# Kernel optimization log

Measured on AMD Instinct MI355X. Metric: run time of the kernel, lower is better.

## Reference

```python
import jax, jax.numpy as jnp
import numpy as np

B, T, D = 2, 1024, 128
NEG_INF = -1e9


def setup_inputs() -> dict:
    key = jax.random.key(0)
    k_h, k_m, k_w = jax.random.split(key, 3)
    h = jax.random.normal(k_h, (B, T, D), dtype=jnp.float32)
    mask = jax.random.uniform(k_m, (B, T)) < 0.9  # bool [B, T]
    w = jax.random.normal(k_w, (D,), dtype=jnp.float32) * (1.0 / np.sqrt(D))  # Linear(dim,1,bias=False)
    return {"h": h, "mask": mask, "w": w}


def reference(h, mask, w):
    # wj[b, j] = W(h[b, j]) : score column scale, independent of i
    wj = jnp.einsum("btd,d->bt", h, w)  # [B, T]
    # pairwise L1 distance: dist[b, i, j] = sum_d |h[b,i,d] - h[b,j,d]|
    dist = jnp.abs(h[:, :, None, :] - h[:, None, :, :]).sum(-1)  # [B, T, T]
    score = -wj[:, None, :] * dist  # [B, T, T]
    score = jnp.where(mask[:, None, :], score, NEG_INF)
    alpha = jax.nn.softmax(score, axis=-1)  # [B, T, T]
    ctx = jnp.einsum("bij,bjd->bid", alpha, h)  # [B, T, D]
    return jnp.concatenate([h, ctx], axis=-1)  # [B, T, 2D]
```

## Files before the change

### kernel.cpp

```cpp
#include <hip/hip_runtime.h>
#include <math.h>

#define TT 1024
#define DD 128

static constexpr float kNegInf = -1e9f;

typedef __fp16 h2 __attribute__((ext_vector_type(2)));

__device__ __forceinline__ unsigned int pk16(float a, float b) {
  h2 v = __builtin_amdgcn_cvt_pkrtz(a, b);
  return __builtin_bit_cast(unsigned int, v);
}
__device__ __forceinline__ float dot2f(unsigned int a, unsigned int b, float c) {
#if __has_builtin(__builtin_amdgcn_fdot2)
  return __builtin_amdgcn_fdot2(__builtin_bit_cast(h2, a),
                                __builtin_bit_cast(h2, b), c, false);
#else
  h2 av = __builtin_bit_cast(h2, a), bv = __builtin_bit_cast(h2, b);
  return c + (float)av.x * (float)bv.x + (float)av.y * (float)bv.y;
#endif
}

__global__ __launch_bounds__(256) void k_prep(const float* __restrict__ h,
                                              const float* __restrict__ w,
                                              const int* __restrict__ mk,
                                              float* __restrict__ hTf,
                                              unsigned int* __restrict__ hT16,
                                              float* __restrict__ swj,
                                              float* __restrict__ bias) {
  __shared__ __align__(16) float tile[32][132];
  __shared__ float wred[32][8];
  const int b  = blockIdx.x >> 5;
  const int jt = blockIdx.x & 31;
  const int tid = threadIdx.x;
  const float4* src = (const float4*)h + (size_t)(b * TT + jt * 32) * 32;
#pragma unroll
  for (int k = 0; k < 4; ++k) {
    int idx = k * 256 + tid;
    float4 v = src[idx];
    int j = idx >> 5, c = idx & 31;
    *((float4*)&tile[j][c * 4]) = v;
  }
  __syncthreads();
#pragma unroll
  for (int k = 0; k < 4; ++k) {
    int idx = k * 256 + tid;
    int d = idx >> 3, jq = idx & 7;
    float4 v = {tile[jq * 4 + 0][d], tile[jq * 4 + 1][d],
                tile[jq * 4 + 2][d], tile[jq * 4 + 3][d]};
    *(float4*)&hTf[(size_t)(b * DD + d) * TT + jt * 32 + jq * 4] = v;
  }
#pragma unroll
  for (int k = 0; k < 2; ++k) {
    int idx = k * 256 + tid;
    int jp = idx >> 5, dq = idx & 31;
    uint4 wv;
    wv.x = pk16(tile[jp * 2][dq * 4 + 0], tile[jp * 2 + 1][dq * 4 + 0]);
    wv.y = pk16(tile[jp * 2][dq * 4 + 1], tile[jp * 2 + 1][dq * 4 + 1]);
    wv.z = pk16(tile[jp * 2][dq * 4 + 2], tile[jp * 2 + 1][dq * 4 + 2]);
    wv.w = pk16(tile[jp * 2][dq * 4 + 3], tile[jp * 2 + 1][dq * 4 + 3]);
    *(uint4*)&hT16[((size_t)(b * 512 + jt * 16 + jp)) * DD + dq * 4] = wv;
  }
  {
    const int j = tid & 31, dg = tid >> 5;
    float p = 0.f;
#pragma unroll
    for (int e = 0; e < 16; e += 4) {
      float4 hv = *(const float4*)&tile[j][dg * 16 + e];
      float4 wv = *(const float4*)&w[dg * 16 + e];
      p += hv.x * wv.x + hv.y * wv.y + hv.z * wv.z + hv.w * wv.w;
    }
    wred[j][dg] = p;
  }
  __syncthreads();
  if (tid < 32) {
    const int row = b * TT + jt * 32 + tid;
    float a = 0.f;
#pragma unroll
    for (int e = 0; e < 8; ++e) a += wred[tid][e];
    const bool ok = (mk[row] != 0);
    swj[row]  = ok ? -a : 0.f;
    bias[row] = ok ? 0.f : kNegInf;
  }
}

__global__ __launch_bounds__(256, 2) void k_fused(
    const float* __restrict__ h, const float* __restrict__ hTf,
    const unsigned int* __restrict__ hT16,
    const float* __restrict__ swj, const float* __restrict__ bias,
    float* __restrict__ out) {
  __shared__ __align__(16) float A_lds[4][DD];
  __shared__ __align__(16) unsigned int Pt[512][4];
  __shared__ __align__(16) float ctxp[4][4][DD];
  __shared__ float redm[4][4];
  __shared__ float redl[4][4];

  const int tid  = threadIdx.x;
  const int lane = tid & 63;
  const int wv   = tid >> 6;
  const int b    = blockIdx.x >> 8;
  const int row0 = (blockIdx.x & 255) * 4;
  const int rot  = blockIdx.x & 31;

  {
    const float2 v = *(const float2*)(h + ((size_t)b * TT + row0) * DD + tid * 2);
    *(float2*)&A_lds[0][tid * 2] = v;
  }
  __syncthreads();

  const int j = tid * 4;
  const float* Bb = hTf + (size_t)b * DD * TT + j;
  float acc[4][4];
#pragma unroll
  for (int u = 0; u < 4; ++u)
#pragma unroll
    for (int r = 0; r < 4; ++r) acc[u][r] = 0.f;

#define PS(s) (((s) + rot) & 31)

#define LOADB4(B, s) {                                        \
    B[0] = *(const float4*)(Bb + (size_t)((s) * 4 + 0) * TT); \
    B[1] = *(const float4*)(Bb + (size_t)((s) * 4 + 1) * TT); \
    B[2] = *(const float4*)(Bb + (size_t)((s) * 4 + 2) * TT); \
    B[3] = *(const float4*)(Bb + (size_t)((s) * 4 + 3) * TT); }

#define COMP4(B, s) {                                                  \
    _Pragma("unroll") for (int r = 0; r < 4; ++r) {                    \
      const float4 Ar = *(const float4*)&A_lds[r][(s) * 4];            \
      _Pragma("unroll") for (int e = 0; e < 4; ++e) {                  \
        const float a = (e == 0) ? Ar.x : (e == 1) ? Ar.y              \
                        : (e == 2) ? Ar.z : Ar.w;                      \
        acc[0][r] += fabsf(a - B[e].x);                                \
        acc[1][r] += fabsf(a - B[e].y);                                \
        acc[2][r] += fabsf(a - B[e].z);                                \
        acc[3][r] += fabsf(a - B[e].w);                                \
      } } }

  {
    float4 B0[4], B1[4];
    LOADB4(B0, PS(0));
#pragma unroll 1
    for (int s = 0; s < 16; ++s) {
      const int p1 = PS(2 * s + 1);
      const int p0 = PS(2 * s);
      LOADB4(B1, p1);
      COMP4(B0, p0);
      if (s < 15) LOADB4(B0, PS(2 * s + 2));
      COMP4(B1, p1);
    }
  }

  const float4 swv = *(const float4*)(swj + (size_t)b * TT + j);
  const float4 bvv = *(const float4*)(bias + (size_t)b * TT + j);
  float sc[4][4];
#pragma unroll
  for (int r = 0; r < 4; ++r) {
    sc[0][r] = fmaf(swv.x, acc[0][r], bvv.x);
    sc[1][r] = fmaf(swv.y, acc[1][r], bvv.y);
    sc[2][r] = fmaf(swv.z, acc[2][r], bvv.z);
    sc[3][r] = fmaf(swv.w, acc[3][r], bvv.w);
  }

  {
    float mr[4];
#pragma unroll
    for (int r = 0; r < 4; ++r) {
      float m0 = fmaxf(fmaxf(sc[0][r], sc[1][r]), fmaxf(sc[2][r], sc[3][r]));
#pragma unroll
      for (int off = 32; off; off >>= 1) m0 = fmaxf(m0, __shfl_xor(m0, off));
      mr[r] = m0;
    }
    if (lane == 0) {
#pragma unroll
      for (int r = 0; r < 4; ++r) redm[wv][r] = mr[r];
    }
  }
  __syncthreads();
  float M[4];
#pragma unroll
  for (int r = 0; r < 4; ++r)
    M[r] = fmaxf(fmaxf(redm[0][r], redm[1][r]),
                 fmaxf(redm[2][r], redm[3][r]));

  {
    float p[4][4];
    float ls[4] = {0.f, 0.f, 0.f, 0.f};
#pragma unroll
    for (int u = 0; u < 4; ++u)
#pragma unroll
      for (int r = 0; r < 4; ++r) {
        p[u][r] = __expf(sc[u][r] - M[r]);
        ls[r] += p[u][r];
      }
    uint4 w0 = {pk16(p[0][0], p[1][0]), pk16(p[0][1], p[1][1]),
                pk16(p[0][2], p[1][2]), pk16(p[0][3], p[1][3])};
    uint4 w1 = {pk16(p[2][0], p[3][0]), pk16(p[2][1], p[3][1]),
                pk16(p[2][2], p[3][2]), pk16(p[2][3], p[3][3])};
    *(uint4*)&Pt[tid * 2 + 0][0] = w0;
    *(uint4*)&Pt[tid * 2 + 1][0] = w1;
#pragma unroll
    for (int r = 0; r < 4; ++r) {
#pragma unroll
      for (int off = 32; off; off >>= 1) ls[r] += __shfl_xor(ls[r], off);
    }
    if (lane == 0) {
#pragma unroll
      for (int r = 0; r < 4; ++r) redl[wv][r] = ls[r];
    }
  }
  __syncthreads();

  const int dp = tid & 63;
  const int s  = tid >> 6;
  const unsigned int* Vp =
      hT16 + ((size_t)(b * 512 + s * 128)) * DD + dp * 2;
  float cx[4][2];
#pragma unroll
  for (int r = 0; r < 4; ++r) { cx[r][0] = 0.f; cx[r][1] = 0.f; }
  const int qrot = rot * 4;
#pragma unroll 4
  for (int qq = 0; qq < 128; ++qq) {
    const int q = (qq + qrot) & 127;
    const uint4 P = *(const uint4*)&Pt[s * 128 + q][0];
    const uint2 V = *(const uint2*)(Vp + (size_t)q * DD);
    cx[0][0] = dot2f(P.x, V.x, cx[0][0]); cx[0][1] = dot2f(P.x, V.y, cx[0][1]);
    cx[1][0] = dot2f(P.y, V.x, cx[1][0]); cx[1][1] = dot2f(P.y, V.y, cx[1][1]);
    cx[2][0] = dot2f(P.z, V.x, cx[2][0]); cx[2][1] = dot2f(P.z, V.y, cx[2][1]);
    cx[3][0] = dot2f(P.w, V.x, cx[3][0]); cx[3][1] = dot2f(P.w, V.y, cx[3][1]);
  }
#pragma unroll
  for (int r = 0; r < 4; ++r)
    *(float2*)&ctxp[s][r][dp * 2] = make_float2(cx[r][0], cx[r][1]);
  __syncthreads();

#pragma unroll
  for (int k = 0; k < 2; ++k) {
    const int idx = tid + k * 256;
    const int r = idx >> 7, d = idx & 127;
    const float L = redl[0][r] + redl[1][r] + redl[2][r] + redl[3][r];
    const float c = (ctxp[0][r][d] + ctxp[1][r][d]) +
                    (ctxp[2][r][d] + ctxp[3][r][d]);
    const size_t row = (size_t)blockIdx.x * 4 + r;
    out[row * 256 + d]       = A_lds[r][d];
    out[row * 256 + 128 + d] = c / L;
  }
}

extern "C" void kernel_launch(void* const* d_in, const int* in_sizes, int n_in,
                              void* d_out, int out_size, void* d_ws, size_t ws_size,
                              hipStream_t stream) {
  const float* h  = (const float*)d_in[0];
  const int*   mk = (const int*)d_in[1];
  const float* w  = (const float*)d_in[2];
  float* out = (float*)d_out;

  char* ws = (char*)d_ws;
  float*        swj  = (float*)ws;
  float*        bias = (float*)(ws + 8192);
  float*        hTf  = (float*)(ws + 16384);
  unsigned int* hT16 = (unsigned int*)(ws + 16384 + 1048576);

  hipLaunchKernelGGL(k_prep,  dim3(64),  dim3(256), 0, stream,
                     h, w, mk, hTf, hT16, swj, bias);
  hipLaunchKernelGGL(k_fused, dim3(512), dim3(256), 0, stream,
                     h, hTf, hT16, swj, bias, out);
}
```

Measured before the change: 41.13 us.

## Split fused kernel to exploit L1-distance symmetry via materialized score matrix

The fused distance-plus-softmax kernel is split into a score kernel and a softmax/context kernel. The score kernel computes only the upper-triangular blocks of the symmetric pairwise L1 distance. It writes both the score and its transpose (scaled by the row weight) into a global TxT score buffer. The softmax kernel then reads scores from that buffer. This roughly halves the distance arithmetic but adds an extra launch and about 8 MB of global writes and reads, plus scattered transposed stores.

```diff
diff --git a/kernel.cpp b/kernel.cpp
--- a/kernel.cpp
+++ b/kernel.cpp
@@ -85,57 +85,59 @@
   }
 }
 
-__global__ __launch_bounds__(256, 2) void k_fused(
+__global__ __launch_bounds__(256) void k_score(
     const float* __restrict__ h, const float* __restrict__ hTf,
-    const unsigned int* __restrict__ hT16,
     const float* __restrict__ swj, const float* __restrict__ bias,
-    float* __restrict__ out) {
+    float* __restrict__ S) {
   __shared__ __align__(16) float A_lds[4][DD];
-  __shared__ __align__(16) unsigned int Pt[512][4];
-  __shared__ __align__(16) float ctxp[4][4][DD];
-  __shared__ float redm[4][4];
-  __shared__ float redl[4][4];
-
-  const int tid  = threadIdx.x;
-  const int lane = tid & 63;
-  const int wv   = tid >> 6;
-  const int b    = blockIdx.x >> 8;
-  const int row0 = (blockIdx.x & 255) * 4;
-  const int rot  = blockIdx.x & 31;
-
-  {
-    const float2 v = *(const float2*)(h + ((size_t)b * TT + row0) * DD + tid * 2);
+
+  const int tid = threadIdx.x;
+  int t = blockIdx.x;
+  const int b = (t >= 384) ? 1 : 0;
+  t -= b * 384;
+  const int jh = (t < 128) ? 0 : 1;
+  const int rp = (t < 128) ? t : (t - 128);
+  const int i0 = rp * 4;
+  const int off = (jh == 0) ? i0 : ((i0 > 512) ? (i0 - 512) : 0);
+  const int jstart = jh * 512 + off;
+  const int nq = (512 - off) >> 2;
+  const int rot = blockIdx.x & 31;
+
+  {
+    const float2 v = *(const float2*)(h + ((size_t)b * TT + i0) * DD + tid * 2);
     *(float2*)&A_lds[0][tid * 2] = v;
   }
   __syncthreads();
 
-  const int j = tid * 4;
+  const int q  = tid & 127;
+  const int g2 = (tid >> 7) * 2;
+  if (q >= nq) return;
+  const int j = jstart + q * 4;
   const float* Bb = hTf + (size_t)b * DD * TT + j;
-  float acc[4][4];
-#pragma unroll
-  for (int u = 0; u < 4; ++u)
-#pragma unroll
-    for (int r = 0; r < 4; ++r) acc[u][r] = 0.f;
+
+  float acc[4][2];
+#pragma unroll
+  for (int u = 0; u < 4; ++u) { acc[u][0] = 0.f; acc[u][1] = 0.f; }
 
 #define PS(s) (((s) + rot) & 31)
-
 #define LOADB4(B, s) {                                        \
     B[0] = *(const float4*)(Bb + (size_t)((s) * 4 + 0) * TT); \
     B[1] = *(const float4*)(Bb + (size_t)((s) * 4 + 1) * TT); \
     B[2] = *(const float4*)(Bb + (size_t)((s) * 4 + 2) * TT); \
     B[3] = *(const float4*)(Bb + (size_t)((s) * 4 + 3) * TT); }
-
-#define COMP4(B, s) {                                                  \
-    _Pragma("unroll") for (int r = 0; r < 4; ++r) {                    \
-      const float4 Ar = *(const float4*)&A_lds[r][(s) * 4];            \
-      _Pragma("unroll") for (int e = 0; e < 4; ++e) {                  \
-        const float a = (e == 0) ? Ar.x : (e == 1) ? Ar.y              \
-                        : (e == 2) ? Ar.z : Ar.w;                      \
-        acc[0][r] += fabsf(a - B[e].x);                                \
-        acc[1][r] += fabsf(a - B[e].y);                                \
-        acc[2][r] += fabsf(a - B[e].z);                                \
-        acc[3][r] += fabsf(a - B[e].w);                                \
-      } } }
+#define COMP2(B, s) {                                                  \
+    const float4 A0 = *(const float4*)&A_lds[g2][(s) * 4];             \
+    const float4 A1 = *(const float4*)&A_lds[g2 + 1][(s) * 4];         \
+    _Pragma("unroll") for (int e = 0; e < 4; ++e) {                    \
+      const float a0 = (e == 0) ? A0.x : (e == 1) ? A0.y               \
+                       : (e == 2) ? A0.z : A0.w;                       \
+      const float a1 = (e == 0) ? A1.x : (e == 1) ? A1.y               \
+                       : (e == 2) ? A1.z : A1.w;                       \
+      acc[0][0] += fabsf(a0 - B[e].x); acc[0][1] += fabsf(a1 - B[e].x);\
+      acc[1][0] += fabsf(a0 - B[e].y); acc[1][1] += fabsf(a1 - B[e].y);\
+      acc[2][0] += fabsf(a0 - B[e].z); acc[2][1] += fabsf(a1 - B[e].z);\
+      acc[3][0] += fabsf(a0 - B[e].w); acc[3][1] += fabsf(a1 - B[e].w);\
+    } }
 
   {
     float4 B0[4], B1[4];
@@ -145,21 +147,66 @@
       const int p1 = PS(2 * s + 1);
       const int p0 = PS(2 * s);
       LOADB4(B1, p1);
-      COMP4(B0, p0);
+      COMP2(B0, p0);
       if (s < 15) LOADB4(B0, PS(2 * s + 2));
-      COMP4(B1, p1);
+      COMP2(B1, p1);
     }
   }
 
   const float4 swv = *(const float4*)(swj + (size_t)b * TT + j);
   const float4 bvv = *(const float4*)(bias + (size_t)b * TT + j);
+  float* Sb = S + (size_t)b * TT * TT;
+#pragma unroll
+  for (int r = 0; r < 2; ++r) {
+    float4 dv;
+    dv.x = fmaf(swv.x, acc[0][r], bvv.x);
+    dv.y = fmaf(swv.y, acc[1][r], bvv.y);
+    dv.z = fmaf(swv.z, acc[2][r], bvv.z);
+    dv.w = fmaf(swv.w, acc[3][r], bvv.w);
+    *(float4*)&Sb[(size_t)(i0 + g2 + r) * TT + j] = dv;
+  }
+  const float swi0 = swj[b * TT + i0 + g2];
+  const float swi1 = swj[b * TT + i0 + g2 + 1];
+  const float bii0 = bias[b * TT + i0 + g2];
+  const float bii1 = bias[b * TT + i0 + g2 + 1];
+#pragma unroll
+  for (int u = 0; u < 4; ++u) {
+    float2 tv;
+    tv.x = fmaf(swi0, acc[u][0], bii0);
+    tv.y = fmaf(swi1, acc[u][1], bii1);
+    *(float2*)&Sb[(size_t)(j + u) * TT + i0 + g2] = tv;
+  }
+}
+
+__global__ __launch_bounds__(256, 2) void k_sm(
+    const float* __restrict__ h, const float* __restrict__ S,
+    const unsigned int* __restrict__ hT16, float* __restrict__ out) {
+  __shared__ __align__(16) float A_lds[4][DD];
+  __shared__ __align__(16) unsigned int Pt[512][4];
+  __shared__ __align__(16) float ctxp[4][4][DD];
+  __shared__ float redm[4][4];
+  __shared__ float redl[4][4];
+
+  const int tid  = threadIdx.x;
+  const int lane = tid & 63;
+  const int wv   = tid >> 6;
+  const int b    = blockIdx.x >> 8;
+  const int row0 = (blockIdx.x & 255) * 4;
+  const int rot  = blockIdx.x & 31;
+
+  {
+    const float2 v = *(const float2*)(h + ((size_t)b * TT + row0) * DD + tid * 2);
+    *(float2*)&A_lds[0][tid * 2] = v;
+  }
+  __syncthreads();
+
+  const int j = tid * 4;
+  const float* Sb = S + ((size_t)b * TT + row0) * TT;
   float sc[4][4];
 #pragma unroll
   for (int r = 0; r < 4; ++r) {
-    sc[0][r] = fmaf(swv.x, acc[0][r], bvv.x);
-    sc[1][r] = fmaf(swv.y, acc[1][r], bvv.y);
-    sc[2][r] = fmaf(swv.z, acc[2][r], bvv.z);
-    sc[3][r] = fmaf(swv.w, acc[3][r], bvv.w);
+    const float4 sv = *(const float4*)&Sb[(size_t)r * TT + j];
+    sc[0][r] = sv.x; sc[1][r] = sv.y; sc[2][r] = sv.z; sc[3][r] = sv.w;
   }
 
   {
@@ -260,9 +307,12 @@
   float*        bias = (float*)(ws + 8192);
   float*        hTf  = (float*)(ws + 16384);
   unsigned int* hT16 = (unsigned int*)(ws + 16384 + 1048576);
+  float*        S    = (float*)(ws + 16384 + 1048576 + 524288);
 
   hipLaunchKernelGGL(k_prep,  dim3(64),  dim3(256), 0, stream,
                      h, w, mk, hTf, hT16, swj, bias);
-  hipLaunchKernelGGL(k_fused, dim3(512), dim3(256), 0, stream,
-                     h, hTf, hT16, swj, bias, out);
-}
+  hipLaunchKernelGGL(k_score, dim3(768), dim3(256), 0, stream,
+                     h, hTf, swj, bias, S);
+  hipLaunchKernelGGL(k_sm,    dim3(512), dim3(256), 0, stream,
+                     h, S, hT16, out);
+}
```

After: 44.43 us. 1.08x slower.
